# Kernel optimization log

Hardware: AMD Instinct MI355X
Metric: run time of the kernel (lower is better)

## Reference

```python
import jax, jax.numpy as jnp
import numpy as np

N_IN, N_HID, N_OUT = 128, 1024, 64
B, T = 128, 256
SIGMA_NEU = 0.05
ALPHA = 0.25

def setup_inputs() -> dict:
    key = jax.random.key(0)
    ks = jax.random.split(key, 6)
    input_signal = jax.random.normal(ks[0], (B, T, N_IN), dtype=jnp.float32)
    hidden = jax.random.normal(ks[1], (B, N_HID), dtype=jnp.float32)
    w_in_w = jax.random.normal(ks[2], (N_HID, N_IN), dtype=jnp.float32) / np.sqrt(N_IN)
    w_hh_w = jax.random.normal(ks[3], (N_HID, N_HID), dtype=jnp.float32) / np.sqrt(N_HID)
    w_hh_b = jnp.zeros((N_HID,), dtype=jnp.float32)
    w_out_w = jax.random.normal(ks[4], (N_OUT, N_HID), dtype=jnp.float32) / np.sqrt(N_HID)
    alpha = jnp.full((N_HID,), ALPHA, dtype=jnp.float32)
    noise_raw = jax.random.normal(ks[5], (B, N_HID), dtype=jnp.float32)
    return {
        'input_signal': input_signal,
        'hidden': hidden,
        'w_in_w': w_in_w,
        'w_hh_w': w_hh_w,
        'w_hh_b': w_hh_b,
        'w_out_w': w_out_w,
        'alpha': alpha,
        'noise_raw': noise_raw,
        'perturbation_timing': 100,
    }

def reference(input_signal, hidden, w_in_w, w_hh_w, w_hh_b, w_out_w, alpha, noise_raw, perturbation_timing):
    # input_signal: [B, T, n_in] -> time-major [T, B, n_in]
    x = jnp.swapaxes(input_signal, 0, 1)
    length = x.shape[0]
    # neural noise injected only at t == perturbation_timing (torch: randn*sigma*sqrt(alpha))
    noise = noise_raw * SIGMA_NEU * jnp.sqrt(alpha)

    def step(h, inp):
        t, x_t = inp
        activated = jnp.tanh(h)
        tmp = x_t @ w_in_w.T + activated @ w_hh_w.T + w_hh_b  # [B, n_hid]
        h_new = (1.0 - alpha) * h + alpha * tmp
        h_new = jnp.where(t == perturbation_timing, h_new + noise, h_new)
        out = h_new @ w_out_w.T  # [B, n_out]
        return h_new, (h_new, out)

    h_final, (hs, outs) = jax.lax.scan(step, hidden, (jnp.arange(length), x))
    hidden_list = jnp.swapaxes(hs, 0, 1)   # [B, T, n_hid]
    output_list = jnp.swapaxes(outs, 0, 1)  # [B, T, n_out]
    return hidden_list, output_list, h_final
```

## Files before the change

kernel.cpp:

```cpp
#include <hip/hip_runtime.h>

typedef _Float16 half8 __attribute__((ext_vector_type(8)));
typedef float floatx4 __attribute__((ext_vector_type(4)));
typedef float floatx2 __attribute__((ext_vector_type(2)));

#define N_IN   128
#define N_HID  1024
#define N_OUT  64
#define BB     128
#define TT     256

#define WHH_STRIDE 1032
#define WIN_STRIDE 136
#define RED_STRIDE 33
#define HSH_STRIDE 40

__device__ __forceinline__ float tanh_fast(float v) {
    float e = __expf(2.0f * v);
    return 1.0f - 2.0f / (e + 1.0f);
}

__global__ __launch_bounds__(256, 1) void rnn_seq_kernel(
    const float* __restrict__ x,
    const float* __restrict__ h0,
    const float* __restrict__ w_in,
    const float* __restrict__ w_hh,
    const float* __restrict__ w_hh_b,
    const float* __restrict__ w_out,
    const float* __restrict__ alpha,
    const float* __restrict__ noise_raw,
    const int* __restrict__ pt_ptr,
    float* __restrict__ out,
    _Float16* __restrict__ actbuf,
    unsigned int* __restrict__ flags)
{
    __shared__ _Float16 Whh_hi[32 * WHH_STRIDE];
    __shared__ _Float16 Whh_lo[32 * WHH_STRIDE];
    __shared__ _Float16 Win_hi[32 * WIN_STRIDE];
    __shared__ _Float16 Win_lo[32 * WIN_STRIDE];
    __shared__ float red[4 * 16 * RED_STRIDE];
    __shared__ _Float16 hsh[16 * HSH_STRIDE];

    const int tid  = threadIdx.x;
    const int bid  = blockIdx.x;
    const int g    = bid & 7;
    const int s    = bid >> 3;
    const int w    = tid >> 6;
    const int lane = tid & 63;
    const int quad = lane >> 4;
    const int mrow = lane & 15;

    for (int p = 0; p < 32; ++p) {
        int f4 = tid + (p << 8);
        int c  = f4 >> 8;
        int k4 = (f4 & 255) << 2;
        floatx4 wv = *(const floatx4*)(w_hh + ((size_t)(s * 32 + c) << 10) + k4);
        #pragma unroll
        for (int i = 0; i < 4; ++i) {
            float v = wv[i];
            _Float16 hi = (_Float16)v;
            _Float16 lo = (_Float16)((v - (float)hi) * 1024.0f);
            Whh_hi[c * WHH_STRIDE + k4 + i] = hi;
            Whh_lo[c * WHH_STRIDE + k4 + i] = lo;
        }
    }
    for (int p = 0; p < 4; ++p) {
        int f4 = tid + (p << 8);
        int c  = f4 >> 5;
        int k4 = (f4 & 31) << 2;
        floatx4 wv = *(const floatx4*)(w_in + ((size_t)(s * 32 + c) << 7) + k4);
        #pragma unroll
        for (int i = 0; i < 4; ++i) {
            float v = wv[i];
            _Float16 hi = (_Float16)v;
            _Float16 lo = (_Float16)((v - (float)hi) * 1024.0f);
            Win_hi[c * WIN_STRIDE + k4 + i] = hi;
            Win_lo[c * WIN_STRIDE + k4 + i] = lo;
        }
    }
    __syncthreads();

    half8 bh0[8], bl0[8], bh1[8], bl1[8];
    #pragma unroll
    for (int kc = 0; kc < 8; ++kc) {
        int kb = (w << 8) + (kc << 5) + (quad << 3);
        bh0[kc] = *(const half8*)&Whh_hi[mrow * WHH_STRIDE + kb];
        bl0[kc] = *(const half8*)&Whh_lo[mrow * WHH_STRIDE + kb];
        bh1[kc] = *(const half8*)&Whh_hi[(16 + mrow) * WHH_STRIDE + kb];
        bl1[kc] = *(const half8*)&Whh_lo[(16 + mrow) * WHH_STRIDE + kb];
    }
    half8 wi_h0, wi_l0, wi_h1, wi_l1;
    {
        int kb = (w << 5) + (quad << 3);
        wi_h0 = *(const half8*)&Win_hi[mrow * WIN_STRIDE + kb];
        wi_l0 = *(const half8*)&Win_lo[mrow * WIN_STRIDE + kb];
        wi_h1 = *(const half8*)&Win_hi[(16 + mrow) * WIN_STRIDE + kb];
        wi_l1 = *(const half8*)&Win_lo[(16 + mrow) * WIN_STRIDE + kb];
    }

    half8 wo;
    {
        const float* wp = w_out + ((size_t)((w << 4) + mrow) << 10) + (s << 5) + (quad << 3);
        floatx4 a0 = *(const floatx4*)wp;
        floatx4 a1 = *(const floatx4*)(wp + 4);
        #pragma unroll
        for (int i = 0; i < 4; ++i) { wo[i] = (_Float16)a0[i]; wo[4 + i] = (_Float16)a1[i]; }
    }

    const int r   = tid >> 4;
    const int c2  = tid & 15;
    const int b   = g * 16 + r;
    const int j0  = s * 32 + 2 * c2;
    const floatx2 a2  = *(const floatx2*)&alpha[j0];
    const floatx2 bi2 = *(const floatx2*)&w_hh_b[j0];
    const floatx2 nr2 = *(const floatx2*)&noise_raw[((size_t)b << 10) + j0];
    const float n0 = nr2.x * 0.05f * __builtin_sqrtf(a2.x);
    const float n1 = nr2.y * 0.05f * __builtin_sqrtf(a2.y);
    const int pt = *pt_ptr;
    floatx2 h2 = *(const floatx2*)&h0[((size_t)b << 10) + j0];
    float hA = h2.x, hB = h2.y;

    float* hidden_list = out;
    float* output_list = out + (size_t)BB * TT * N_HID;
    float* h_final = out + (size_t)BB * TT * N_HID + (size_t)BB * TT * N_OUT;

    {
        unsigned int* act1_32 = (unsigned int*)(actbuf + BB * N_HID);
        union { _Float16 h[2]; unsigned int u; } pk;
        pk.h[0] = (_Float16)tanh_fast(hA);
        pk.h[1] = (_Float16)tanh_fast(hB);
        __hip_atomic_store(&act1_32[(((unsigned)b << 10) + j0) >> 1], pk.u,
                           __ATOMIC_RELAXED, __HIP_MEMORY_SCOPE_AGENT);

        unsigned long long* zb = (unsigned long long*)
            (output_list + ((size_t)b * TT + (s << 3)) * 64 + (c2 << 5));
        #pragma unroll
        for (int i = 0; i < 16; ++i)
            __hip_atomic_store(zb + i, 0ull, __ATOMIC_RELAXED,
                               __HIP_MEMORY_SCOPE_AGENT);
    }
    __syncthreads();
    if (tid == 0)
        __hip_atomic_store(&flags[((unsigned)g) * 32u + s], 1u,
                           __ATOMIC_RELAXED, __HIP_MEMORY_SCOPE_AGENT);

    const int arow = g * 16 + mrow;

    for (int t = 0; t < TT; ++t) {
        const float* xp = x + (((size_t)arow << 8) + t) * N_IN + (w << 5) + (quad << 3);
        floatx4 xf0 = *(const floatx4*)xp;
        floatx4 xf1 = *(const floatx4*)(xp + 4);

        {
            const unsigned tok = (unsigned)t + 1u;
            const unsigned fidx = ((unsigned)t * 8u + g) * 32u + (w << 3) + (lane & 7);
            while (true) {
                unsigned v = __hip_atomic_load(&flags[fidx], __ATOMIC_RELAXED,
                                               __HIP_MEMORY_SCOPE_AGENT);
                if (__ballot(v == tok) == ~0ull) break;
            }
        }

        half8 afr[8];
        {
            const unsigned long long* actq = (const unsigned long long*)
                (actbuf + (size_t)((t & 1) ^ 1) * (BB * N_HID));
            const unsigned long long* p =
                actq + ((((size_t)arow << 10) + (w << 8) + (quad << 3)) >> 2);
            #pragma unroll
            for (int kc = 0; kc < 8; ++kc) {
                union { unsigned long long u[2]; half8 h; } cv;
                cv.u[0] = __hip_atomic_load(p + kc * 8,     __ATOMIC_RELAXED,
                                            __HIP_MEMORY_SCOPE_AGENT);
                cv.u[1] = __hip_atomic_load(p + kc * 8 + 1, __ATOMIC_RELAXED,
                                            __HIP_MEMORY_SCOPE_AGENT);
                afr[kc] = cv.h;
            }
        }
        half8 xfr;
        #pragma unroll
        for (int i = 0; i < 4; ++i) { xfr[i] = (_Float16)xf0[i]; xfr[4 + i] = (_Float16)xf1[i]; }

        floatx4 acch0 = {0.f,0.f,0.f,0.f}, acch1 = {0.f,0.f,0.f,0.f};
        floatx4 accl0 = {0.f,0.f,0.f,0.f}, accl1 = {0.f,0.f,0.f,0.f};

        acch0 = __builtin_amdgcn_mfma_f32_16x16x32_f16(xfr, wi_h0, acch0, 0, 0, 0);
        accl0 = __builtin_amdgcn_mfma_f32_16x16x32_f16(xfr, wi_l0, accl0, 0, 0, 0);
        acch1 = __builtin_amdgcn_mfma_f32_16x16x32_f16(xfr, wi_h1, acch1, 0, 0, 0);
        accl1 = __builtin_amdgcn_mfma_f32_16x16x32_f16(xfr, wi_l1, accl1, 0, 0, 0);

        #pragma unroll
        for (int kc = 0; kc < 8; ++kc) {
            acch0 = __builtin_amdgcn_mfma_f32_16x16x32_f16(afr[kc], bh0[kc], acch0, 0, 0, 0);
            accl0 = __builtin_amdgcn_mfma_f32_16x16x32_f16(afr[kc], bl0[kc], accl0, 0, 0, 0);
            acch1 = __builtin_amdgcn_mfma_f32_16x16x32_f16(afr[kc], bh1[kc], acch1, 0, 0, 0);
            accl1 = __builtin_amdgcn_mfma_f32_16x16x32_f16(afr[kc], bl1[kc], accl1, 0, 0, 0);
        }

        #pragma unroll
        for (int rr = 0; rr < 4; ++rr) {
            red[(w * 16 + quad * 4 + rr) * RED_STRIDE + mrow]
                = acch0[rr] + accl0[rr] * (1.0f / 1024.0f);
            red[(w * 16 + quad * 4 + rr) * RED_STRIDE + 16 + mrow]
                = acch1[rr] + accl1[rr] * (1.0f / 1024.0f);
        }
        __syncthreads();

        float t0v = bi2.x, t1v = bi2.y;
        #pragma unroll
        for (int ww = 0; ww < 4; ++ww) {
            t0v += red[(ww * 16 + r) * RED_STRIDE + 2 * c2];
            t1v += red[(ww * 16 + r) * RED_STRIDE + 2 * c2 + 1];
        }
        hA = (1.0f - a2.x) * hA + a2.x * t0v;
        hB = (1.0f - a2.y) * hB + a2.y * t1v;
        if (t == pt) { hA += n0; hB += n1; }

        {
            union { _Float16 h[2]; unsigned int u; } pk, pk2;
            pk.h[0]  = (_Float16)tanh_fast(hA);
            pk.h[1]  = (_Float16)tanh_fast(hB);
            unsigned int* actw32 = (unsigned int*)(actbuf + (size_t)(t & 1) * (BB * N_HID));
            __hip_atomic_store(&actw32[(((unsigned)b << 10) + j0) >> 1], pk.u,
                               __ATOMIC_RELAXED, __HIP_MEMORY_SCOPE_AGENT);
            pk2.h[0] = (_Float16)hA;
            pk2.h[1] = (_Float16)hB;
            ((unsigned int*)hsh)[r * (HSH_STRIDE / 2) + c2] = pk2.u;
        }

        __syncthreads();
        if (tid == 0)
            __hip_atomic_store(&flags[((unsigned)(t + 1) * 8u + g) * 32u + s],
                               (unsigned)t + 2u,
                               __ATOMIC_RELAXED, __HIP_MEMORY_SCOPE_AGENT);


        floatx2 hv = {hA, hB};
        *(floatx2*)&hidden_list[(((size_t)b << 8) + t) * N_HID + j0] = hv;

        {
            half8 ha = *(const half8*)&hsh[mrow * HSH_STRIDE + (quad << 3)];
            floatx4 aco = {0.f,0.f,0.f,0.f};
            aco = __builtin_amdgcn_mfma_f32_16x16x32_f16(ha, wo, aco, 0, 0, 0);
            #pragma unroll
            for (int rr = 0; rr < 4; ++rr)
                atomicAdd(&output_list[((size_t)(g * 16 + quad * 4 + rr) * TT + t) * 64
                                       + (w << 4) + mrow], aco[rr]);
        }
    }

    *(floatx2*)&h_final[((size_t)b << 10) + j0] = (floatx2){hA, hB};
}

extern "C" void kernel_launch(void* const* d_in, const int* in_sizes, int n_in,
                              void* d_out, int out_size, void* d_ws, size_t ws_size,
                              hipStream_t stream)
{
    const float* x      = (const float*)d_in[0];
    const float* h0     = (const float*)d_in[1];
    const float* w_in   = (const float*)d_in[2];
    const float* w_hh   = (const float*)d_in[3];
    const float* w_hh_b = (const float*)d_in[4];
    const float* w_out  = (const float*)d_in[5];
    const float* alpha  = (const float*)d_in[6];
    const float* noise  = (const float*)d_in[7];
    const int*   pt     = (const int*)d_in[8];
    float* out = (float*)d_out;

    _Float16* actbuf = (_Float16*)d_ws;
    unsigned int* flags =
        (unsigned int*)((char*)d_ws + (size_t)2 * BB * N_HID * sizeof(_Float16));

    hipLaunchKernelGGL(rnn_seq_kernel, dim3(256), dim3(256), 0, stream,
                       x, h0, w_in, w_hh, w_hh_b, w_out, alpha, noise, pt, out,
                       actbuf, flags);
}
```

Measured before the change: 1.123 ms.

## Replace per-step flag handshake with tagged activation words polled directly

Each fp16 activation pair is packed into a 64-bit word with a step tag in the upper half. Consumers poll the activation data itself and retry only the words that are still stale, instead of spinning on per-block flags and then loading the data. This drops the producer-side barrier-then-flag publish and the separate flag wait. Full __syncthreads are replaced by an LDS-only wait plus s_barrier, so global stores no longer have to drain at each barrier. In exchange, activation traffic doubles, and correctness depends on each tagged 64-bit store and load being atomic.

```diff
diff --git a/kernel.cpp b/kernel.cpp
--- a/kernel.cpp
+++ b/kernel.cpp
@@ -31,8 +31,7 @@
     const float* __restrict__ noise_raw,
     const int* __restrict__ pt_ptr,
     float* __restrict__ out,
-    _Float16* __restrict__ actbuf,
-    unsigned int* __restrict__ flags)
+    unsigned long long* __restrict__ actu)
 {
     __shared__ _Float16 Whh_hi[32 * WHH_STRIDE];
     __shared__ _Float16 Whh_lo[32 * WHH_STRIDE];
@@ -77,34 +76,6 @@
             Win_hi[c * WIN_STRIDE + k4 + i] = hi;
             Win_lo[c * WIN_STRIDE + k4 + i] = lo;
         }
-    }
-    __syncthreads();
-
-    half8 bh0[8], bl0[8], bh1[8], bl1[8];
-    #pragma unroll
-    for (int kc = 0; kc < 8; ++kc) {
-        int kb = (w << 8) + (kc << 5) + (quad << 3);
-        bh0[kc] = *(const half8*)&Whh_hi[mrow * WHH_STRIDE + kb];
-        bl0[kc] = *(const half8*)&Whh_lo[mrow * WHH_STRIDE + kb];
-        bh1[kc] = *(const half8*)&Whh_hi[(16 + mrow) * WHH_STRIDE + kb];
-        bl1[kc] = *(const half8*)&Whh_lo[(16 + mrow) * WHH_STRIDE + kb];
-    }
-    half8 wi_h0, wi_l0, wi_h1, wi_l1;
-    {
-        int kb = (w << 5) + (quad << 3);
-        wi_h0 = *(const half8*)&Win_hi[mrow * WIN_STRIDE + kb];
-        wi_l0 = *(const half8*)&Win_lo[mrow * WIN_STRIDE + kb];
-        wi_h1 = *(const half8*)&Win_hi[(16 + mrow) * WIN_STRIDE + kb];
-        wi_l1 = *(const half8*)&Win_lo[(16 + mrow) * WIN_STRIDE + kb];
-    }
-
-    half8 wo;
-    {
-        const float* wp = w_out + ((size_t)((w << 4) + mrow) << 10) + (s << 5) + (quad << 3);
-        floatx4 a0 = *(const floatx4*)wp;
-        floatx4 a1 = *(const floatx4*)(wp + 4);
-        #pragma unroll
-        for (int i = 0; i < 4; ++i) { wo[i] = (_Float16)a0[i]; wo[4 + i] = (_Float16)a1[i]; }
     }
 
     const int r   = tid >> 4;
@@ -125,13 +96,6 @@
     float* h_final = out + (size_t)BB * TT * N_HID + (size_t)BB * TT * N_OUT;
 
     {
-        unsigned int* act1_32 = (unsigned int*)(actbuf + BB * N_HID);
-        union { _Float16 h[2]; unsigned int u; } pk;
-        pk.h[0] = (_Float16)tanh_fast(hA);
-        pk.h[1] = (_Float16)tanh_fast(hB);
-        __hip_atomic_store(&act1_32[(((unsigned)b << 10) + j0) >> 1], pk.u,
-                           __ATOMIC_RELAXED, __HIP_MEMORY_SCOPE_AGENT);
-
         unsigned long long* zb = (unsigned long long*)
             (output_list + ((size_t)b * TT + (s << 3)) * 64 + (c2 << 5));
         #pragma unroll
@@ -140,9 +104,42 @@
                                __HIP_MEMORY_SCOPE_AGENT);
     }
     __syncthreads();
-    if (tid == 0)
-        __hip_atomic_store(&flags[((unsigned)g) * 32u + s], 1u,
-                           __ATOMIC_RELAXED, __HIP_MEMORY_SCOPE_AGENT);
+
+    half8 bh0[8], bl0[8], bh1[8], bl1[8];
+    #pragma unroll
+    for (int kc = 0; kc < 8; ++kc) {
+        int kb = (w << 8) + (kc << 5) + (quad << 3);
+        bh0[kc] = *(const half8*)&Whh_hi[mrow * WHH_STRIDE + kb];
+        bl0[kc] = *(const half8*)&Whh_lo[mrow * WHH_STRIDE + kb];
+        bh1[kc] = *(const half8*)&Whh_hi[(16 + mrow) * WHH_STRIDE + kb];
+        bl1[kc] = *(const half8*)&Whh_lo[(16 + mrow) * WHH_STRIDE + kb];
+    }
+    half8 wi_h0, wi_l0, wi_h1, wi_l1;
+    {
+        int kb = (w << 5) + (quad << 3);
+        wi_h0 = *(const half8*)&Win_hi[mrow * WIN_STRIDE + kb];
+        wi_l0 = *(const half8*)&Win_lo[mrow * WIN_STRIDE + kb];
+        wi_h1 = *(const half8*)&Win_hi[(16 + mrow) * WIN_STRIDE + kb];
+        wi_l1 = *(const half8*)&Win_lo[(16 + mrow) * WIN_STRIDE + kb];
+    }
+
+    half8 wo;
+    {
+        const float* wp = w_out + ((size_t)((w << 4) + mrow) << 10) + (s << 5) + (quad << 3);
+        floatx4 a0 = *(const floatx4*)wp;
+        floatx4 a1 = *(const floatx4*)(wp + 4);
+        #pragma unroll
+        for (int i = 0; i < 4; ++i) { wo[i] = (_Float16)a0[i]; wo[4 + i] = (_Float16)a1[i]; }
+    }
+
+    {
+        union { _Float16 h[2]; unsigned u; } pk;
+        pk.h[0] = (_Float16)tanh_fast(hA);
+        pk.h[1] = (_Float16)tanh_fast(hB);
+        unsigned long long e = (1ull << 32) | (unsigned long long)pk.u;
+        __hip_atomic_store(&actu[(size_t)(BB * 512) + ((unsigned)b << 9) + (s << 4) + c2],
+                           e, __ATOMIC_RELAXED, __HIP_MEMORY_SCOPE_AGENT);
+    }
 
     const int arow = g * 16 + mrow;
 
@@ -151,32 +148,40 @@
         floatx4 xf0 = *(const floatx4*)xp;
         floatx4 xf1 = *(const floatx4*)(xp + 4);
 
-        {
-            const unsigned tok = (unsigned)t + 1u;
-            const unsigned fidx = ((unsigned)t * 8u + g) * 32u + (w << 3) + (lane & 7);
-            while (true) {
-                unsigned v = __hip_atomic_load(&flags[fidx], __ATOMIC_RELAXED,
-                                               __HIP_MEMORY_SCOPE_AGENT);
-                if (__ballot(v == tok) == ~0ull) break;
+        const unsigned tok = (unsigned)t + 1u;
+        const unsigned long long* pbase =
+            actu + (size_t)((t & 1) ^ 1) * (BB * 512) + ((size_t)arow << 9) + (w << 7);
+        union AV { half8 h; unsigned u[4]; } af[8];
+        unsigned miss = 0;
+        #pragma unroll
+        for (int kc = 0; kc < 8; ++kc) {
+            #pragma unroll
+            for (int i = 0; i < 4; ++i) {
+                unsigned long long v = __hip_atomic_load(
+                    pbase + (kc << 4) + (quad << 2) + i,
+                    __ATOMIC_RELAXED, __HIP_MEMORY_SCOPE_AGENT);
+                af[kc].u[i] = (unsigned)v;
+                if ((unsigned)(v >> 32) != tok) miss |= (1u << (kc * 4 + i));
             }
         }
-
-        half8 afr[8];
-        {
-            const unsigned long long* actq = (const unsigned long long*)
-                (actbuf + (size_t)((t & 1) ^ 1) * (BB * N_HID));
-            const unsigned long long* p =
-                actq + ((((size_t)arow << 10) + (w << 8) + (quad << 3)) >> 2);
+        while (__ballot(miss != 0)) {
             #pragma unroll
             for (int kc = 0; kc < 8; ++kc) {
-                union { unsigned long long u[2]; half8 h; } cv;
-                cv.u[0] = __hip_atomic_load(p + kc * 8,     __ATOMIC_RELAXED,
-                                            __HIP_MEMORY_SCOPE_AGENT);
-                cv.u[1] = __hip_atomic_load(p + kc * 8 + 1, __ATOMIC_RELAXED,
-                                            __HIP_MEMORY_SCOPE_AGENT);
-                afr[kc] = cv.h;
+                #pragma unroll
+                for (int i = 0; i < 4; ++i) {
+                    if (miss & (1u << (kc * 4 + i))) {
+                        unsigned long long v = __hip_atomic_load(
+                            pbase + (kc << 4) + (quad << 2) + i,
+                            __ATOMIC_RELAXED, __HIP_MEMORY_SCOPE_AGENT);
+                        if ((unsigned)(v >> 32) == tok) {
+                            af[kc].u[i] = (unsigned)v;
+                            miss &= ~(1u << (kc * 4 + i));
+                        }
+                    }
+                }
             }
         }
+
         half8 xfr;
         #pragma unroll
         for (int i = 0; i < 4; ++i) { xfr[i] = (_Float16)xf0[i]; xfr[4 + i] = (_Float16)xf1[i]; }
@@ -191,10 +196,10 @@
 
         #pragma unroll
         for (int kc = 0; kc < 8; ++kc) {
-            acch0 = __builtin_amdgcn_mfma_f32_16x16x32_f16(afr[kc], bh0[kc], acch0, 0, 0, 0);
-            accl0 = __builtin_amdgcn_mfma_f32_16x16x32_f16(afr[kc], bl0[kc], accl0, 0, 0, 0);
-            acch1 = __builtin_amdgcn_mfma_f32_16x16x32_f16(afr[kc], bh1[kc], acch1, 0, 0, 0);
-            accl1 = __builtin_amdgcn_mfma_f32_16x16x32_f16(afr[kc], bl1[kc], accl1, 0, 0, 0);
+            acch0 = __builtin_amdgcn_mfma_f32_16x16x32_f16(af[kc].h, bh0[kc], acch0, 0, 0, 0);
+            accl0 = __builtin_amdgcn_mfma_f32_16x16x32_f16(af[kc].h, bl0[kc], accl0, 0, 0, 0);
+            acch1 = __builtin_amdgcn_mfma_f32_16x16x32_f16(af[kc].h, bh1[kc], acch1, 0, 0, 0);
+            accl1 = __builtin_amdgcn_mfma_f32_16x16x32_f16(af[kc].h, bl1[kc], accl1, 0, 0, 0);
         }
 
         #pragma unroll
@@ -204,7 +209,8 @@
             red[(w * 16 + quad * 4 + rr) * RED_STRIDE + 16 + mrow]
                 = acch1[rr] + accl1[rr] * (1.0f / 1024.0f);
         }
-        __syncthreads();
+        asm volatile("s_waitcnt lgkmcnt(0)" ::: "memory");
+        __builtin_amdgcn_s_barrier();
 
         float t0v = bi2.x, t1v = bi2.y;
         #pragma unroll
@@ -217,26 +223,28 @@
         if (t == pt) { hA += n0; hB += n1; }
 
         {
-            union { _Float16 h[2]; unsigned int u; } pk, pk2;
-            pk.h[0]  = (_Float16)tanh_fast(hA);
-            pk.h[1]  = (_Float16)tanh_fast(hB);
-            unsigned int* actw32 = (unsigned int*)(actbuf + (size_t)(t & 1) * (BB * N_HID));
-            __hip_atomic_store(&actw32[(((unsigned)b << 10) + j0) >> 1], pk.u,
+            union { _Float16 h[2]; unsigned u; } pk;
+            pk.h[0] = (_Float16)tanh_fast(hA);
+            pk.h[1] = (_Float16)tanh_fast(hB);
+            unsigned long long e = ((unsigned long long)(t + 2u) << 32)
+                                 | (unsigned long long)pk.u;
+            unsigned long long* actw = actu + (size_t)(t & 1) * (BB * 512);
+            __hip_atomic_store(&actw[((unsigned)b << 9) + (s << 4) + c2], e,
                                __ATOMIC_RELAXED, __HIP_MEMORY_SCOPE_AGENT);
+        }
+
+
+        {
+            union { _Float16 h[2]; unsigned u; } pk2;
             pk2.h[0] = (_Float16)hA;
             pk2.h[1] = (_Float16)hB;
             ((unsigned int*)hsh)[r * (HSH_STRIDE / 2) + c2] = pk2.u;
         }
-
-        __syncthreads();
-        if (tid == 0)
-            __hip_atomic_store(&flags[((unsigned)(t + 1) * 8u + g) * 32u + s],
-                               (unsigned)t + 2u,
-                               __ATOMIC_RELAXED, __HIP_MEMORY_SCOPE_AGENT);
-
-
         floatx2 hv = {hA, hB};
         *(floatx2*)&hidden_list[(((size_t)b << 8) + t) * N_HID + j0] = hv;
+
+        asm volatile("s_waitcnt lgkmcnt(0)" ::: "memory");
+        __builtin_amdgcn_s_barrier();
 
         {
             half8 ha = *(const half8*)&hsh[mrow * HSH_STRIDE + (quad << 3)];
@@ -267,11 +275,9 @@
     const int*   pt     = (const int*)d_in[8];
     float* out = (float*)d_out;
 
-    _Float16* actbuf = (_Float16*)d_ws;
-    unsigned int* flags =
-        (unsigned int*)((char*)d_ws + (size_t)2 * BB * N_HID * sizeof(_Float16));
+    unsigned long long* actu = (unsigned long long*)d_ws;
 
     hipLaunchKernelGGL(rnn_seq_kernel, dim3(256), dim3(256), 0, stream,
                        x, h0, w_in, w_hh, w_hh_b, w_out, alpha, noise, pt, out,
-                       actbuf, flags);
+                       actu);
 }
```

Result: slower. 1.747 ms (+55.6%).

## Use XCD-local cached activation exchange when all producer blocks share an XCD

Applied to the files above, without the earlier changes.

Each block now records its XCD id in the startup flag. At t==0 every wave checks whether all producers of its activation slice sit on the same XCD. If they do, the per-step activation reads switch to vector dwordx4 loads with sc0 and the writes become plain stores, instead of 64-bit agent-scope atomic loads and atomic stores. This is meant to cut the latency of the inter-block activation exchange through the shared L2, but it relies on XCD placement and cache coherence assumptions that may not hold, and if the blocks are spread across XCDs the old path still runs.

```diff
diff --git a/kernel.cpp b/kernel.cpp
--- a/kernel.cpp
+++ b/kernel.cpp
@@ -18,6 +18,12 @@
 __device__ __forceinline__ float tanh_fast(float v) {
     float e = __expf(2.0f * v);
     return 1.0f - 2.0f / (e + 1.0f);
+}
+
+__device__ __forceinline__ half8 load_b128_sc0(const _Float16* p) {
+    half8 r;
+    asm volatile("global_load_dwordx4 %0, %1, off sc0" : "=v"(r) : "v"(p));
+    return r;
 }
 
 __global__ __launch_bounds__(256, 1) void rnn_seq_kernel(
@@ -40,6 +46,7 @@
     __shared__ _Float16 Win_lo[32 * WIN_STRIDE];
     __shared__ float red[4 * 16 * RED_STRIDE];
     __shared__ _Float16 hsh[16 * HSH_STRIDE];
+    __shared__ unsigned ptab[4];
 
     const int tid  = threadIdx.x;
     const int bid  = blockIdx.x;
@@ -49,6 +56,8 @@
     const int lane = tid & 63;
     const int quad = lane >> 4;
     const int mrow = lane & 15;
+
+    const unsigned myxcd = __builtin_amdgcn_s_getreg(63508) & 0xfu;
 
     for (int p = 0; p < 32; ++p) {
         int f4 = tid + (p << 8);
@@ -141,10 +150,12 @@
     }
     __syncthreads();
     if (tid == 0)
-        __hip_atomic_store(&flags[((unsigned)g) * 32u + s], 1u,
+        __hip_atomic_store(&flags[((unsigned)g) * 32u + s],
+                           1u | (myxcd << 8),
                            __ATOMIC_RELAXED, __HIP_MEMORY_SCOPE_AGENT);
 
     const int arow = g * 16 + mrow;
+    bool l2m = false;
 
     for (int t = 0; t < TT; ++t) {
         const float* xp = x + (((size_t)arow << 8) + t) * N_IN + (w << 5) + (quad << 3);
@@ -154,15 +165,29 @@
         {
             const unsigned tok = (unsigned)t + 1u;
             const unsigned fidx = ((unsigned)t * 8u + g) * 32u + (w << 3) + (lane & 7);
+            unsigned v;
             while (true) {
-                unsigned v = __hip_atomic_load(&flags[fidx], __ATOMIC_RELAXED,
-                                               __HIP_MEMORY_SCOPE_AGENT);
-                if (__ballot(v == tok) == ~0ull) break;
+                v = __hip_atomic_load(&flags[fidx], __ATOMIC_RELAXED,
+                                      __HIP_MEMORY_SCOPE_AGENT);
+                bool got = (t == 0) ? ((v & 0xffu) == 1u) : (v == tok);
+                if (__ballot(got) == ~0ull) break;
             }
+            if (t == 0) {
+                unsigned long long bb = __ballot((v >> 8) == myxcd);
+                if (lane == 0) ptab[w] = (bb == ~0ull) ? 1u : 0u;
+            }
         }
 
         half8 afr[8];
-        {
+        if (l2m) {
+            const _Float16* ab = actbuf + (size_t)((t & 1) ^ 1) * (BB * N_HID)
+                               + ((size_t)arow << 10) + (w << 8) + (quad << 3);
+            #pragma unroll
+            for (int kc = 0; kc < 8; ++kc)
+                afr[kc] = load_b128_sc0(ab + (kc << 5));
+            asm volatile("s_waitcnt vmcnt(0)" ::: "memory");
+            __builtin_amdgcn_sched_barrier(0);
+        } else {
             const unsigned long long* actq = (const unsigned long long*)
                 (actbuf + (size_t)((t & 1) ^ 1) * (BB * N_HID));
             const unsigned long long* p =
@@ -177,6 +202,7 @@
                 afr[kc] = cv.h;
             }
         }
+
         half8 xfr;
         #pragma unroll
         for (int i = 0; i < 4; ++i) { xfr[i] = (_Float16)xf0[i]; xfr[4 + i] = (_Float16)xf1[i]; }
@@ -206,6 +232,9 @@
         }
         __syncthreads();
 
+        if (t == 0)
+            l2m = (ptab[0] & ptab[1] & ptab[2] & ptab[3]) != 0u;
+
         float t0v = bi2.x, t1v = bi2.y;
         #pragma unroll
         for (int ww = 0; ww < 4; ++ww) {
@@ -221,8 +250,10 @@
             pk.h[0]  = (_Float16)tanh_fast(hA);
             pk.h[1]  = (_Float16)tanh_fast(hB);
             unsigned int* actw32 = (unsigned int*)(actbuf + (size_t)(t & 1) * (BB * N_HID));
-            __hip_atomic_store(&actw32[(((unsigned)b << 10) + j0) >> 1], pk.u,
-                               __ATOMIC_RELAXED, __HIP_MEMORY_SCOPE_AGENT);
+            const unsigned idx = (((unsigned)b << 10) + j0) >> 1;
+            if (l2m) actw32[idx] = pk.u;
+            else __hip_atomic_store(&actw32[idx], pk.u,
+                                    __ATOMIC_RELAXED, __HIP_MEMORY_SCOPE_AGENT);
             pk2.h[0] = (_Float16)hA;
             pk2.h[1] = (_Float16)hB;
             ((unsigned int*)hsh)[r * (HSH_STRIDE / 2) + c2] = pk2.u;
```

Measured after the change: 1.067 ms. -5.0%, faster.
